# Performance work log

Hardware: AMD Instinct MI355X
Metric: run time of the kernel (lower is better)

## Reference

```python
import jax, jax.numpy as jnp
import numpy as np

N = 1_000_000  # in_features (number of scalar samples)
M = 128        # number of tanh basis functions; weight has shape [2*M, 1]


def setup_inputs() -> dict:
    key = jax.random.key(0)
    k1, k2 = jax.random.split(key)
    x = jax.random.normal(k1, (N, 1), dtype=jnp.float32)
    # reset_parameters: uniform(-1, 1) since weight.size(1) == 1
    weight = jax.random.uniform(k2, (2 * M, 1), dtype=jnp.float32, minval=-1.0, maxval=1.0)
    return {"input": x, "weight": weight}


def reference(input, weight):
    # ret[i] = sum_k weight[2k] * tanh(input[i] + weight[2k+1])
    amp = weight[0::2, 0]   # [M] amplitudes (even indices)
    bias = weight[1::2, 0]  # [M] biases (odd indices)
    # [N,1] + [M] -> [N,M] tanh, contract over M -> [N]
    out = jnp.tanh(input + bias[None, :]) @ amp
    return out[:, None]  # [N,1]
```

## Files before the change

kernel.cpp:

```cpp
#include <hip/hip_runtime.h>
#include <math.h>

#define M_CNT 128
#define TBLF  128
#define XMIN  (-6.0f)
#define INVH  (10.583333333f)
#define HSTEP (0.0944881886f)
#define TMAX  (126.999f)

__global__ __launch_bounds__(256) void fused_tanh_table_kernel(
        const float* __restrict__ x, float* __restrict__ out,
        const float* __restrict__ w, int n) {
    __shared__ float2 lw[M_CNT];
    __shared__ float  part[2][TBLF];
    __shared__ float2 tbl[TBLF];

    const int tid  = threadIdx.x;
    const int nvec = n >> 2;
    const int rem  = n & 3;

    const float4* xv = (const float4*)x;
    const int i0 = blockIdx.x * 512 + tid;
    const int i1 = i0 + 256;
    float4 v0, v1;
    const bool p0 = i0 < nvec, p1 = i1 < nvec;
    if (p0) v0 = xv[i0];
    if (p1) v1 = xv[i1];

    if (tid < M_CNT) {
        float2 wj = ((const float2*)w)[tid];
        lw[tid] = make_float2(__expf(2.0f * wj.y), wj.x);
    }
    __syncthreads();

    {
        const int e = tid & (TBLF - 1);
        const int p = tid >> 7;
        const float xe = XMIN + (float)e * HSTEP;
        const float E  = __expf(2.0f * xe);
        const float2* lwp = lw + p * 64;
        float acc = 0.0f, sa = 0.0f;
#pragma unroll 8
        for (int j = 0; j < 64; ++j) {
            float2 t = lwp[j];
            float r = __builtin_amdgcn_rcpf(fmaf(E, t.x, 1.0f));
            acc = fmaf(t.y, r, acc);
            sa += t.y;
        }
        part[p][e] = fmaf(-2.0f, acc, sa);
    }
    __syncthreads();

    if (tid < TBLF - 1) {
        float ft  = part[0][tid]     + part[1][tid];
        float ft1 = part[0][tid + 1] + part[1][tid + 1];
        tbl[tid] = make_float2(ft, ft1 - ft);
    }
    __syncthreads();

    float4* ov = (float4*)out;
    if (p0) {
        float4 o;
        float* vp = (float*)&v0; float* op = (float*)&o;
#pragma unroll
        for (int k = 0; k < 4; ++k) {
            float t = (vp[k] - XMIN) * INVH;
            t = fminf(fmaxf(t, 0.0f), TMAX);
            int ii = (int)t;
            float fr = t - (float)ii;
            float2 e = tbl[ii];
            op[k] = fmaf(fr, e.y, e.x);
        }
        ov[i0] = o;
    }
    if (p1) {
        float4 o;
        float* vp = (float*)&v1; float* op = (float*)&o;
#pragma unroll
        for (int k = 0; k < 4; ++k) {
            float t = (vp[k] - XMIN) * INVH;
            t = fminf(fmaxf(t, 0.0f), TMAX);
            int ii = (int)t;
            float fr = t - (float)ii;
            float2 e = tbl[ii];
            op[k] = fmaf(fr, e.y, e.x);
        }
        ov[i1] = o;
    }
    if (blockIdx.x == 0 && tid < rem) {
        int i = nvec * 4 + tid;
        float t = (x[i] - XMIN) * INVH;
        t = fminf(fmaxf(t, 0.0f), TMAX);
        int ii = (int)t;
        float fr = t - (float)ii;
        float2 e = tbl[ii];
        out[i] = fmaf(fr, e.y, e.x);
    }
}

extern "C" void kernel_launch(void* const* d_in, const int* in_sizes, int n_in,
                              void* d_out, int out_size, void* d_ws, size_t ws_size,
                              hipStream_t stream) {
    const float* x = (const float*)d_in[0];
    const float* w = (const float*)d_in[1];
    float* out = (float*)d_out;
    int n = in_sizes[0];

    int nvec = n >> 2;
    int grid = (nvec + 511) / 512;
    if (grid < 1) grid = 1;
    fused_tanh_table_kernel<<<grid, 256, 0, stream>>>(x, out, w, n);
}
```

Baseline: 10.03 us.

## Halve per-block tanh table size and use nontemporal loads/stores

Shrinks the per-block lookup table from 128 to 64 entries and splits the 128-term reduction four ways, so each thread evaluates 32 terms instead of 64 before the table is built. This cuts the per-block prologue that every block repeats. The input loads and output stores also become nontemporal vector accesses to avoid cache pollution on the streaming data. The coarser table spacing increases linear-interpolation error, which may break the accuracy tolerance.

Result: no change. 10.06 us (+0.2%).

```diff
diff --git a/kernel.cpp b/kernel.cpp
--- a/kernel.cpp
+++ b/kernel.cpp
@@ -2,30 +2,32 @@
 #include <math.h>
 
 #define M_CNT 128
-#define TBLF  128
+#define TBLF  64
 #define XMIN  (-6.0f)
-#define INVH  (10.583333333f)
-#define HSTEP (0.0944881886f)
-#define TMAX  (126.999f)
+#define INVH  (5.25f)
+#define HSTEP (0.1904761905f)
+#define TMAX  (62.999f)
+
+typedef float f32x4 __attribute__((ext_vector_type(4)));
 
 __global__ __launch_bounds__(256) void fused_tanh_table_kernel(
         const float* __restrict__ x, float* __restrict__ out,
         const float* __restrict__ w, int n) {
     __shared__ float2 lw[M_CNT];
-    __shared__ float  part[2][TBLF];
+    __shared__ float  part[4][TBLF];
     __shared__ float2 tbl[TBLF];
 
     const int tid  = threadIdx.x;
     const int nvec = n >> 2;
     const int rem  = n & 3;
 
-    const float4* xv = (const float4*)x;
+    const f32x4* xv = (const f32x4*)x;
     const int i0 = blockIdx.x * 512 + tid;
     const int i1 = i0 + 256;
-    float4 v0, v1;
+    f32x4 v0, v1;
     const bool p0 = i0 < nvec, p1 = i1 < nvec;
-    if (p0) v0 = xv[i0];
-    if (p1) v1 = xv[i1];
+    if (p0) v0 = __builtin_nontemporal_load(xv + i0);
+    if (p1) v1 = __builtin_nontemporal_load(xv + i1);
 
     if (tid < M_CNT) {
         float2 wj = ((const float2*)w)[tid];
@@ -35,13 +37,13 @@
 
     {
         const int e = tid & (TBLF - 1);
-        const int p = tid >> 7;
+        const int p = tid >> 6;
         const float xe = XMIN + (float)e * HSTEP;
         const float E  = __expf(2.0f * xe);
-        const float2* lwp = lw + p * 64;
+        const float2* lwp = lw + p * 32;
         float acc = 0.0f, sa = 0.0f;
 #pragma unroll 8
-        for (int j = 0; j < 64; ++j) {
+        for (int j = 0; j < 32; ++j) {
             float2 t = lwp[j];
             float r = __builtin_amdgcn_rcpf(fmaf(E, t.x, 1.0f));
             acc = fmaf(t.y, r, acc);
@@ -52,40 +54,40 @@
     __syncthreads();
 
     if (tid < TBLF - 1) {
-        float ft  = part[0][tid]     + part[1][tid];
-        float ft1 = part[0][tid + 1] + part[1][tid + 1];
+        float ft  = (part[0][tid]     + part[1][tid])
+                  + (part[2][tid]     + part[3][tid]);
+        float ft1 = (part[0][tid + 1] + part[1][tid + 1])
+                  + (part[2][tid + 1] + part[3][tid + 1]);
         tbl[tid] = make_float2(ft, ft1 - ft);
     }
     __syncthreads();
 
-    float4* ov = (float4*)out;
+    f32x4* ov = (f32x4*)out;
     if (p0) {
-        float4 o;
-        float* vp = (float*)&v0; float* op = (float*)&o;
+        f32x4 o;
 #pragma unroll
         for (int k = 0; k < 4; ++k) {
-            float t = (vp[k] - XMIN) * INVH;
+            float t = (v0[k] - XMIN) * INVH;
             t = fminf(fmaxf(t, 0.0f), TMAX);
             int ii = (int)t;
             float fr = t - (float)ii;
             float2 e = tbl[ii];
-            op[k] = fmaf(fr, e.y, e.x);
+            o[k] = fmaf(fr, e.y, e.x);
         }
-        ov[i0] = o;
+        __builtin_nontemporal_store(o, ov + i0);
     }
     if (p1) {
-        float4 o;
-        float* vp = (float*)&v1; float* op = (float*)&o;
+        f32x4 o;
 #pragma unroll
         for (int k = 0; k < 4; ++k) {
-            float t = (vp[k] - XMIN) * INVH;
+            float t = (v1[k] - XMIN) * INVH;
             t = fminf(fmaxf(t, 0.0f), TMAX);
             int ii = (int)t;
             float fr = t - (float)ii;
             float2 e = tbl[ii];
-            op[k] = fmaf(fr, e.y, e.x);
+            o[k] = fmaf(fr, e.y, e.x);
         }
-        ov[i1] = o;
+        __builtin_nontemporal_store(o, ov + i1);
     }
     if (blockIdx.x == 0 && tid < rem) {
         int i = nvec * 4 + tid;
```
